# Kernel optimization log

Measured on AMD Instinct MI355X. Metric: run time of the kernel, lower is better.

Reference implementation:

```python
import jax, jax.numpy as jnp
import numpy as np

TEMP = 0.07
LAM = 0.1
S, Q, P, D = 128, 64, 64, 256


def _l2norm(x):
    # torch F.normalize(p=2, eps=1e-12)
    n = jnp.linalg.norm(x, axis=-1, keepdims=True)
    return x / jnp.maximum(n, 1e-12)


def setup_inputs() -> dict:
    key = jax.random.key(0)
    k1, k2, k3, k4 = jax.random.split(key, 4)
    return {
        "article_title_embedding": jax.random.normal(k1, (1, D), jnp.float32),
        "section_title_embeddings": jax.random.normal(k2, (S, D), jnp.float32),
        "question_embeddings": jax.random.normal(k3, (S, Q, D), jnp.float32),
        "sentence_embeddings": jax.random.normal(k4, (S, P, D), jnp.float32),
    }


def reference(article_title_embedding, section_title_embeddings,
              question_embeddings, sentence_embeddings):
    qn = _l2norm(question_embeddings)   # [S,Q,D]
    sn = _l2norm(sentence_embeddings)   # [S,P,D]
    sn_flat = sn.reshape(-1, sn.shape[-1])  # [S*P, D] all sentences in article
    N_e = sn_flat.shape[0]

    # --- qs_loss: question -> own-section sentences positive, other sections negative ---
    pos_sim = jnp.einsum('sqd,spd->sqp', qn, sn)          # [S,Q,P]
    pos = jnp.exp(pos_sim / TEMP)                          # [S,Q,P]
    all_sim = jnp.einsum('sqd,md->sqm', qn, sn_flat)      # [S,Q,S*P]
    total_exp = jnp.sum(jnp.exp(all_sim / TEMP), axis=-1)  # [S,Q]
    own_exp = jnp.sum(pos, axis=-1)                        # [S,Q]
    neg_sum_exp = total_exp - own_exp                      # sum over other sections

    term1 = -LAM * pos + neg_sum_exp[..., None] / (1.0 - LAM)
    term2 = jnp.exp(jnp.float32(-1.0 / TEMP)) * jnp.float32(N_e - 1)
    N_g = jnp.clip(jnp.maximum(term1, term2), 1e-8, None)
    qs_loss = jnp.sum(-jnp.log(pos / (pos + N_g)))

    # --- sq_loss: section title -> own-section questions positive ---
    stn = _l2norm(section_title_embeddings)                # [S,D]
    pos_q = jnp.exp(jnp.einsum('sd,sqd->sq', stn, qn) / TEMP)  # [S,Q]
    numerator = jnp.sum(pos_q, axis=-1)                    # [S]
    all_q = jnp.exp(jnp.einsum('sd,tqd->stq', stn, qn) / TEMP)  # [S,S,Q]
    denominator = jnp.sum(all_q, axis=(1, 2))              # numerator + negatives
    sq_loss = jnp.sum(-jnp.log(numerator / denominator))

    # --- at_loss: article title vs section titles (no negatives -> 0, kept faithful) ---
    an = _l2norm(article_title_embedding)                  # [1,D]
    at_num = jnp.sum(jnp.exp((an @ stn.T) / TEMP))
    at_loss = -jnp.log(at_num / at_num)

    return qs_loss + sq_loss + at_loss
```

## Files before the change

### kernel.cpp

```cpp
#include <hip/hip_runtime.h>
#include <math.h>

#define S_DIM 128
#define Q_DIM 64
#define P_DIM 64
#define D_DIM 256
#define NQ (S_DIM * Q_DIM)
#define NS (S_DIM * P_DIM)

typedef __attribute__((ext_vector_type(4))) float f32x4;
typedef __attribute__((ext_vector_type(8))) short bf16x8;
typedef __attribute__((ext_vector_type(8))) _Float16 f16x8;
typedef __attribute__((ext_vector_type(4))) _Float16 f16x4;

__device__ __forceinline__ unsigned short f2bf(float f) {
    unsigned int u = __float_as_uint(f);
    u = (u + 0x7fffu + ((u >> 16) & 1u)) >> 16;
    return (unsigned short)u;
}
__device__ __forceinline__ float bf2f(unsigned short h) {
    return __uint_as_float(((unsigned int)h) << 16);
}
__device__ __forceinline__ void gload_lds16(const void* g, void* l) {
    __builtin_amdgcn_global_load_lds(
        (const __attribute__((address_space(1))) void*)g,
        (__attribute__((address_space(3))) void*)l, 16, 0, 0);
}


__global__ __launch_bounds__(256) void normsplit_kernel(
    const float* __restrict__ qm, const float* __restrict__ sm,
    const float* __restrict__ st, float* __restrict__ zero_region,
    _Float16* __restrict__ qf, _Float16* __restrict__ sf, _Float16* __restrict__ stf,
    unsigned short* __restrict__ q_hi, unsigned short* __restrict__ q_lo,
    unsigned short* __restrict__ s_hi, unsigned short* __restrict__ s_lo) {
    if (blockIdx.x < 34) {
        int i = blockIdx.x * 256 + threadIdx.x;
        if (i < 8456) zero_region[i] = 0.0f;
    }
    int row = blockIdx.x * 4 + (threadIdx.x >> 6);
    int lane = threadIdx.x & 63;
    const float* src;
    _Float16* fdst;
    unsigned short *hi = nullptr, *lo = nullptr;
    int r;
    if (row < NQ) {
        r = row; src = qm + (size_t)r * D_DIM; fdst = qf + (size_t)r * D_DIM;
        hi = q_hi + (size_t)r * D_DIM; lo = q_lo + (size_t)r * D_DIM;
    } else if (row < NQ + NS) {
        r = row - NQ; src = sm + (size_t)r * D_DIM; fdst = sf + (size_t)r * D_DIM;
        hi = s_hi + (size_t)r * D_DIM; lo = s_lo + (size_t)r * D_DIM;
    } else if (row < NQ + NS + S_DIM) {
        r = row - NQ - NS; src = st + (size_t)r * D_DIM; fdst = stf + (size_t)r * D_DIM;
    } else return;

    float4 v = reinterpret_cast<const float4*>(src)[lane];
    float ss = v.x * v.x + v.y * v.y + v.z * v.z + v.w * v.w;
    #pragma unroll
    for (int off = 32; off; off >>= 1) ss += __shfl_xor(ss, off);
    float inv = 1.0f / fmaxf(sqrtf(ss), 1e-12f);

    const float CF = sqrtf((1.0f / 0.07f) * 1.44269504088896f);
    float sc = inv * CF;
    float x[4] = {v.x * sc, v.y * sc, v.z * sc, v.w * sc};

    f16x4 fv;
    #pragma unroll
    for (int e = 0; e < 4; e++) fv[e] = (_Float16)x[e];
    reinterpret_cast<f16x4*>(fdst)[lane] = fv;

    if (hi) {
        ushort4 h, l;
        unsigned short* hp = &h.x; unsigned short* lp = &l.x;
        #pragma unroll
        for (int e = 0; e < 4; e++) {
            unsigned short hh = f2bf(x[e]);
            hp[e] = hh;
            lp[e] = f2bf(x[e] - bf2f(hh));
        }
        reinterpret_cast<ushort4*>(hi)[lane] = h;
        reinterpret_cast<ushort4*>(lo)[lane] = l;
    }
}

__global__ __launch_bounds__(512, 4) void mfma_stream_kernel(
    const _Float16* __restrict__ qf, const _Float16* __restrict__ sf,
    const _Float16* __restrict__ stf,
    float* __restrict__ total_exp, float* __restrict__ den, float* __restrict__ num) {
    __shared__ __align__(16) char lds[2][32768];
    const int tid = threadIdx.x;
    const int wid = tid >> 6, lane = tid & 63;
    const int lane15 = lane & 15, kg = lane >> 4;
    const int wr = wid >> 1, wc = wid & 1;

    const bool cpass = (blockIdx.x < 64);
    const _Float16* A;
    const _Float16* B;
    int row0, colbase, ntiles;
    if (cpass) {
        A = stf; B = qf; row0 = 0;
        colbase = (int)blockIdx.x * 128; ntiles = 2;
    } else {
        const int b = (int)blockIdx.x - 64;
        A = qf; B = sf;
        row0 = (b >> 3) * 128;
        colbase = (b & 7) * 1024;
        ntiles = 16;
    }

    f16x8 af[2][8];
    {
        const _Float16* ap = A + (((size_t)(row0 + wr * 32 + lane15)) << 8) + kg * 8;
        #pragma unroll
        for (int mb = 0; mb < 2; mb++)
            #pragma unroll
            for (int c = 0; c < 8; c++)
                af[mb][c] = *reinterpret_cast<const f16x8*>(ap + mb * 16 * 256 + c * 32);
    }

    auto STAGE = [&](int buf, int t) {
        const _Float16* src = B + (((size_t)(colbase + t * 64 + lane)) << 8) + wid * 32;
        #pragma unroll
        for (int i = 0; i < 4; i++)
            gload_lds16(src + i * 8, &lds[buf][0] + wid * 4096 + i * 1024);
    };

    float rs[2][4] = {{0.f, 0.f, 0.f, 0.f}, {0.f, 0.f, 0.f, 0.f}};
    float nm[2][4] = {{0.f, 0.f, 0.f, 0.f}, {0.f, 0.f, 0.f, 0.f}};

    STAGE(0, 0);
    __syncthreads();

    for (int t = 0; t < ntiles; t++) {
        if (t + 1 < ntiles) STAGE((t + 1) & 1, t + 1);
        const char* Bb = &lds[t & 1][0];

        f32x4 acc[2][2];
        #pragma unroll
        for (int mb = 0; mb < 2; mb++)
            #pragma unroll
            for (int n = 0; n < 2; n++) acc[mb][n] = (f32x4){0.f, 0.f, 0.f, 0.f};

        #pragma unroll
        for (int c = 0; c < 8; c++) {
            f16x8 bf[2];
            #pragma unroll
            for (int n = 0; n < 2; n++)
                bf[n] = *reinterpret_cast<const f16x8*>(
                    Bb + c * 4096 + kg * 1024 + (wc * 32 + n * 16 + lane15) * 16);
            #pragma unroll
            for (int mb = 0; mb < 2; mb++)
                #pragma unroll
                for (int n = 0; n < 2; n++)
                    acc[mb][n] = __builtin_amdgcn_mfma_f32_16x16x32_f16(
                        af[mb][c], bf[n], acc[mb][n], 0, 0, 0);
        }

        #pragma unroll
        for (int mb = 0; mb < 2; mb++)
            #pragma unroll
            for (int j = 0; j < 4; j++) {
                const int grow = row0 + wr * 32 + mb * 16 + kg * 4 + j;
                #pragma unroll
                for (int n = 0; n < 2; n++) {
                    float e = exp2f(acc[mb][n][j]);
                    rs[mb][j] += e;
                    if (cpass) {
                        int col = colbase + t * 64 + wc * 32 + n * 16 + lane15;
                        if ((col >> 6) == grow) nm[mb][j] += e;
                    }
                }
            }
        __syncthreads();
    }

    #pragma unroll
    for (int mb = 0; mb < 2; mb++)
        #pragma unroll
        for (int j = 0; j < 4; j++) {
            float v = rs[mb][j], w = nm[mb][j];
            #pragma unroll
            for (int off = 1; off < 16; off <<= 1) {
                v += __shfl_xor(v, off);
                if (cpass) w += __shfl_xor(w, off);
            }
            if (lane15 == 0) {
                const int grow = row0 + wr * 32 + mb * 16 + kg * 4 + j;
                if (cpass) {
                    atomicAdd(&den[grow], v);
                    atomicAdd(&num[grow], w);
                } else {
                    atomicAdd(&total_exp[grow], v);
                }
            }
        }
}

__global__ __launch_bounds__(128) void qs2_kernel(
    const unsigned short* __restrict__ q_hi, const unsigned short* __restrict__ q_lo,
    const unsigned short* __restrict__ s_hi, const unsigned short* __restrict__ s_lo,
    const float* __restrict__ total_exp, const float* __restrict__ den,
    const float* __restrict__ num, double* __restrict__ loss_acc,
    unsigned int* __restrict__ ticket, float* __restrict__ out) {
    const int s = blockIdx.x >> 1;
    const int tid = threadIdx.x;
    const int wid2 = ((blockIdx.x & 1) << 1) + (tid >> 6);
    const int lane = tid & 63;
    __shared__ double wsum[2];
    __shared__ float w2[2];
    __shared__ unsigned int winner_s;

    const int arow = s * 64 + wid2 * 16 + (lane & 15);
    const int koff = (lane >> 4) * 8;

    bf16x8 ah[8], al[8];
    #pragma unroll
    for (int k8 = 0; k8 < 8; k8++) {
        ah[k8] = *reinterpret_cast<const bf16x8*>(&q_hi[(size_t)arow * D_DIM + k8 * 32 + koff]);
        al[k8] = *reinterpret_cast<const bf16x8*>(&q_lo[(size_t)arow * D_DIM + k8 * 32 + koff]);
    }

    f32x4 acc[4];
    #pragma unroll
    for (int n = 0; n < 4; n++) acc[n] = (f32x4){0.f, 0.f, 0.f, 0.f};
    #pragma unroll
    for (int n = 0; n < 4; n++) {
        const int brow = s * 64 + n * 16 + (lane & 15);
        #pragma unroll
        for (int k8 = 0; k8 < 8; k8++) {
            bf16x8 bh = *reinterpret_cast<const bf16x8*>(&s_hi[(size_t)brow * D_DIM + k8 * 32 + koff]);
            bf16x8 bl = *reinterpret_cast<const bf16x8*>(&s_lo[(size_t)brow * D_DIM + k8 * 32 + koff]);
            acc[n] = __builtin_amdgcn_mfma_f32_16x16x32_bf16(ah[k8], bh, acc[n], 0, 0, 0);
            acc[n] = __builtin_amdgcn_mfma_f32_16x16x32_bf16(ah[k8], bl, acc[n], 0, 0, 0);
            acc[n] = __builtin_amdgcn_mfma_f32_16x16x32_bf16(al[k8], bh, acc[n], 0, 0, 0);
        }
    }

    const float term2 = expf(-1.0f / 0.07f) * (float)(NS - 1);
    double lacc = 0.0;
    #pragma unroll
    for (int j = 0; j < 4; j++) {
        float e[4];
        float part = 0.0f;
        #pragma unroll
        for (int n = 0; n < 4; n++) { e[n] = exp2f(acc[n][j]); part += e[n]; }
        #pragma unroll
        for (int off = 1; off < 16; off <<= 1) part += __shfl_xor(part, off);
        const int trow = s * 64 + wid2 * 16 + (lane >> 4) * 4 + j;
        const float neg = total_exp[trow] - part;
        #pragma unroll
        for (int n = 0; n < 4; n++) {
            float posv = e[n];
            float t1 = fmaf(-0.1f, posv, neg / 0.9f);
            float Ng = fmaxf(fmaxf(t1, term2), 1e-8f);
            lacc += (double)(-logf(posv / (posv + Ng)));
        }
    }
    #pragma unroll
    for (int off = 1; off < 64; off <<= 1) lacc += __shfl_xor(lacc, off);
    if (lane == 0) wsum[tid >> 6] = lacc;
    __syncthreads();
    if (tid == 0) {
        atomicAdd(loss_acc, wsum[0] + wsum[1]);
        __threadfence();
        winner_s = atomicAdd(ticket, 1u);
    }
    __syncthreads();
    if (winner_s == 255) {
        __threadfence();
        float l = -logf(num[tid] / den[tid]);
        #pragma unroll
        for (int off = 1; off < 64; off <<= 1) l += __shfl_xor(l, off);
        if ((tid & 63) == 0) w2[tid >> 6] = l;
        __syncthreads();
        if (tid == 0) out[0] = (float)(loss_acc[0] + (double)(w2[0] + w2[1]));
    }
}

extern "C" void kernel_launch(void* const* d_in, const int* in_sizes, int n_in,
                              void* d_out, int out_size, void* d_ws, size_t ws_size,
                              hipStream_t stream) {
    const float* st = (const float*)d_in[1];
    const float* qm = (const float*)d_in[2];
    const float* sm = (const float*)d_in[3];

    float* ws        = (float*)d_ws;
    float* total_exp = ws;
    float* den       = ws + 8192;
    float* num       = ws + 8320;
    double* loss_acc = (double*)(ws + 8448);
    unsigned int* ticket = (unsigned int*)(ws + 8452);
    _Float16* fbase = (_Float16*)(ws + 8704);
    _Float16* qf  = fbase;
    _Float16* sf  = fbase + 2097152;
    _Float16* stf = fbase + 4194304;
    unsigned short* b16 = (unsigned short*)fbase;
    unsigned short* q_hi = b16 + 4718592;
    unsigned short* q_lo = b16 + 6815744;
    unsigned short* s_hi = b16 + 8912896;
    unsigned short* s_lo = b16 + 11010048;
    float* out = (float*)d_out;

    hipLaunchKernelGGL(normsplit_kernel, dim3(4128), dim3(256), 0, stream,
                       qm, sm, st, ws, qf, sf, stf, q_hi, q_lo, s_hi, s_lo);
    hipLaunchKernelGGL(mfma_stream_kernel, dim3(576), dim3(512), 0, stream,
                       qf, sf, stf, total_exp, den, num);
    hipLaunchKernelGGL(qs2_kernel, dim3(256), dim3(128), 0, stream,
                       q_hi, q_lo, s_hi, s_lo, total_exp, den, num,
                       loss_acc, ticket, out);
}
```

Baseline: 158.0 us.

## Stream B operands directly from global/L2 into registers, dropping LDS staging

Replaces the LDS double-buffered B-tile staging (global_load_lds plus per-tile __syncthreads) with direct per-wave global loads of B fragments, relying on L2 for reuse. Each wave now owns a 64-row A block held in registers and walks its own column panel independently, with a new block/grid decomposition (256 threads, 544 blocks). This removes the barrier and LDS traffic but increases global/L2 load volume and register pressure from the larger A fragment arrays.

```diff
diff --git a/kernel.cpp b/kernel.cpp
--- a/kernel.cpp
+++ b/kernel.cpp
@@ -20,11 +20,6 @@
 }
 __device__ __forceinline__ float bf2f(unsigned short h) {
     return __uint_as_float(((unsigned int)h) << 16);
-}
-__device__ __forceinline__ void gload_lds16(const void* g, void* l) {
-    __builtin_amdgcn_global_load_lds(
-        (const __attribute__((address_space(1))) void*)g,
-        (__attribute__((address_space(3))) void*)l, 16, 0, 0);
 }
 
 
@@ -83,112 +78,101 @@
     }
 }
 
-__global__ __launch_bounds__(512, 4) void mfma_stream_kernel(
+__global__ __launch_bounds__(256, 2) void mfma_l2stream_kernel(
     const _Float16* __restrict__ qf, const _Float16* __restrict__ sf,
     const _Float16* __restrict__ stf,
     float* __restrict__ total_exp, float* __restrict__ den, float* __restrict__ num) {
-    __shared__ __align__(16) char lds[2][32768];
     const int tid = threadIdx.x;
-    const int wid = tid >> 6, lane = tid & 63;
+    const int w = tid >> 6, lane = tid & 63;
     const int lane15 = lane & 15, kg = lane >> 4;
-    const int wr = wid >> 1, wc = wid & 1;
-
-    const bool cpass = (blockIdx.x < 64);
+
+    const bool cpass = (blockIdx.x < 32);
     const _Float16* A;
     const _Float16* B;
-    int row0, colbase, ntiles;
+    int row0, colbase, nG;
     if (cpass) {
-        A = stf; B = qf; row0 = 0;
-        colbase = (int)blockIdx.x * 128; ntiles = 2;
+        const int idx = (int)blockIdx.x * 4 + w;
+        A = stf; B = qf;
+        row0 = (idx >> 6) * 64;
+        colbase = (idx & 63) * 128;
+        nG = 4;
     } else {
-        const int b = (int)blockIdx.x - 64;
+        const int b2 = (int)blockIdx.x - 32;
         A = qf; B = sf;
-        row0 = (b >> 3) * 128;
-        colbase = (b & 7) * 1024;
-        ntiles = 16;
-    }
-
-    f16x8 af[2][8];
+        const int panel = (b2 & 7) * 2 + (w & 1);
+        const int rg = (b2 >> 3) * 2 + (w >> 1);
+        row0 = rg * 64;
+        colbase = panel * 512;
+        nG = 16;
+    }
+
+    f16x8 af[4][8];
     {
-        const _Float16* ap = A + (((size_t)(row0 + wr * 32 + lane15)) << 8) + kg * 8;
-        #pragma unroll
-        for (int mb = 0; mb < 2; mb++)
+        const _Float16* ap = A + (((size_t)(row0 + lane15)) << 8) + kg * 8;
+        #pragma unroll
+        for (int mb = 0; mb < 4; mb++)
             #pragma unroll
             for (int c = 0; c < 8; c++)
                 af[mb][c] = *reinterpret_cast<const f16x8*>(ap + mb * 16 * 256 + c * 32);
     }
 
-    auto STAGE = [&](int buf, int t) {
-        const _Float16* src = B + (((size_t)(colbase + t * 64 + lane)) << 8) + wid * 32;
-        #pragma unroll
-        for (int i = 0; i < 4; i++)
-            gload_lds16(src + i * 8, &lds[buf][0] + wid * 4096 + i * 1024);
-    };
-
-    float rs[2][4] = {{0.f, 0.f, 0.f, 0.f}, {0.f, 0.f, 0.f, 0.f}};
-    float nm[2][4] = {{0.f, 0.f, 0.f, 0.f}, {0.f, 0.f, 0.f, 0.f}};
-
-    STAGE(0, 0);
-    __syncthreads();
-
-    for (int t = 0; t < ntiles; t++) {
-        if (t + 1 < ntiles) STAGE((t + 1) & 1, t + 1);
-        const char* Bb = &lds[t & 1][0];
-
-        f32x4 acc[2][2];
-        #pragma unroll
-        for (int mb = 0; mb < 2; mb++)
-            #pragma unroll
-            for (int n = 0; n < 2; n++) acc[mb][n] = (f32x4){0.f, 0.f, 0.f, 0.f};
-
+    float rs[4][4] = {{0.f}}, nm[4][4] = {{0.f}};
+    #pragma unroll
+    for (int mb = 0; mb < 4; mb++)
+        #pragma unroll
+        for (int j = 0; j < 4; j++) { rs[mb][j] = 0.f; nm[mb][j] = 0.f; }
+
+    const _Float16* bp = B + (((size_t)(colbase + lane15)) << 8) + kg * 8;
+
+    for (int ct = 0; ct < nG; ct++) {
+        f32x4 acc[4][2];
+        #pragma unroll
+        for (int mb = 0; mb < 4; mb++) {
+            acc[mb][0] = (f32x4){0.f, 0.f, 0.f, 0.f};
+            acc[mb][1] = (f32x4){0.f, 0.f, 0.f, 0.f};
+        }
+        const _Float16* bpc = bp + (size_t)ct * 32 * 256;
         #pragma unroll
         for (int c = 0; c < 8; c++) {
-            f16x8 bf[2];
-            #pragma unroll
-            for (int n = 0; n < 2; n++)
-                bf[n] = *reinterpret_cast<const f16x8*>(
-                    Bb + c * 4096 + kg * 1024 + (wc * 32 + n * 16 + lane15) * 16);
-            #pragma unroll
-            for (int mb = 0; mb < 2; mb++)
-                #pragma unroll
-                for (int n = 0; n < 2; n++)
-                    acc[mb][n] = __builtin_amdgcn_mfma_f32_16x16x32_f16(
-                        af[mb][c], bf[n], acc[mb][n], 0, 0, 0);
-        }
-
-        #pragma unroll
-        for (int mb = 0; mb < 2; mb++)
+            f16x8 bf0 = *reinterpret_cast<const f16x8*>(bpc + c * 32);
+            f16x8 bf1 = *reinterpret_cast<const f16x8*>(bpc + 16 * 256 + c * 32);
+            #pragma unroll
+            for (int mb = 0; mb < 4; mb++) {
+                acc[mb][0] = __builtin_amdgcn_mfma_f32_16x16x32_f16(af[mb][c], bf0, acc[mb][0], 0, 0, 0);
+                acc[mb][1] = __builtin_amdgcn_mfma_f32_16x16x32_f16(af[mb][c], bf1, acc[mb][1], 0, 0, 0);
+            }
+        }
+        #pragma unroll
+        for (int mb = 0; mb < 4; mb++)
             #pragma unroll
             for (int j = 0; j < 4; j++) {
-                const int grow = row0 + wr * 32 + mb * 16 + kg * 4 + j;
-                #pragma unroll
-                for (int n = 0; n < 2; n++) {
-                    float e = exp2f(acc[mb][n][j]);
-                    rs[mb][j] += e;
-                    if (cpass) {
-                        int col = colbase + t * 64 + wc * 32 + n * 16 + lane15;
-                        if ((col >> 6) == grow) nm[mb][j] += e;
-                    }
+                float e0 = exp2f(acc[mb][0][j]);
+                float e1 = exp2f(acc[mb][1][j]);
+                rs[mb][j] += e0 + e1;
+                if (cpass) {
+                    const int grow = row0 + mb * 16 + kg * 4 + j;
+                    const int c0 = colbase + ct * 32 + lane15;
+                    if ((c0 >> 6) == grow) nm[mb][j] += e0;
+                    if (((c0 + 16) >> 6) == grow) nm[mb][j] += e1;
                 }
             }
-        __syncthreads();
-    }
-
-    #pragma unroll
-    for (int mb = 0; mb < 2; mb++)
+    }
+
+    #pragma unroll
+    for (int mb = 0; mb < 4; mb++)
         #pragma unroll
         for (int j = 0; j < 4; j++) {
-            float v = rs[mb][j], w = nm[mb][j];
+            float v = rs[mb][j], u = nm[mb][j];
             #pragma unroll
             for (int off = 1; off < 16; off <<= 1) {
                 v += __shfl_xor(v, off);
-                if (cpass) w += __shfl_xor(w, off);
+                if (cpass) u += __shfl_xor(u, off);
             }
             if (lane15 == 0) {
-                const int grow = row0 + wr * 32 + mb * 16 + kg * 4 + j;
+                const int grow = row0 + mb * 16 + kg * 4 + j;
                 if (cpass) {
                     atomicAdd(&den[grow], v);
-                    atomicAdd(&num[grow], w);
+                    atomicAdd(&num[grow], u);
                 } else {
                     atomicAdd(&total_exp[grow], v);
                 }
@@ -303,7 +287,7 @@
 
     hipLaunchKernelGGL(normsplit_kernel, dim3(4128), dim3(256), 0, stream,
                        qm, sm, st, ws, qf, sf, stf, q_hi, q_lo, s_hi, s_lo);
-    hipLaunchKernelGGL(mfma_stream_kernel, dim3(576), dim3(512), 0, stream,
+    hipLaunchKernelGGL(mfma_l2stream_kernel, dim3(544), dim3(256), 0, stream,
                        qf, sf, stf, total_exp, den, num);
     hipLaunchKernelGGL(qs2_kernel, dim3(256), dim3(128), 0, stream,
                        q_hi, q_lo, s_hi, s_lo, total_exp, den, num,
```

After: 184.1 us. +16.5%, slower.
